# Kernel optimization log

Hardware: AMD Instinct MI355X
Metric: run time of the kernel (lower is better)

Reference implementation:

```python
import jax, jax.numpy as jnp
import numpy as np

KS = 16
FREQ = jnp.array([0., 1., 2., 4., 8., 16., 32., 64.], dtype=jnp.float32)  # [0]+[2^i], d=8
TWO_PI = 2.0 * np.pi


def softplus_b10(x):
    # torch F.softplus(x, beta=10, threshold=1): linear when beta*x > threshold
    bx = 10.0 * x
    return jnp.where(bx > 1.0, x, jnp.log1p(jnp.exp(jnp.minimum(bx, 1.0))) / 10.0)


def grid_sample_2d(img, gx, gy):
    # img: (C, H, W) complex; gx,gy: (N,) in [-1,1]. Bilinear, align_corners=True,
    # zero padding -- matches torch.nn.functional.grid_sample. Returns (C, N).
    C, H, W = img.shape
    ix = (gx + 1.0) * 0.5 * (W - 1)
    iy = (gy + 1.0) * 0.5 * (H - 1)
    ix0 = jnp.floor(ix)
    iy0 = jnp.floor(iy)
    wx = ix - ix0
    wy = iy - iy0

    def corner(iyc, ixc, w):
        valid = (ixc >= 0) & (ixc <= W - 1) & (iyc >= 0) & (iyc <= H - 1)
        ii = jnp.clip(ixc, 0, W - 1).astype(jnp.int32)
        jj = jnp.clip(iyc, 0, H - 1).astype(jnp.int32)
        return img[:, jj, ii] * (w * valid)[None, :]

    return (corner(iy0, ix0, (1 - wx) * (1 - wy))
            + corner(iy0, ix0 + 1, wx * (1 - wy))
            + corner(iy0 + 1, ix0, (1 - wx) * wy)
            + corner(iy0 + 1, ix0 + 1, wx * wy))


def batch_irfft(P, x):
    # P: (ks, d, N) complex; x: (N,) in [-1,1]. Trig-weighted inverse rFFT reduce.
    xx = (x + 1.0) * 0.5
    ang = TWO_PI * xx[:, None] * FREQ[None, :]            # (N, d)
    scale = jnp.where(FREQ > 0, 2.0, 1.0)
    c = jnp.cos(ang) * scale
    s = jnp.sin(ang) * scale
    return jnp.einsum('kdn,nd->kn', P.real, c) - jnp.einsum('kdn,nd->kn', P.imag, s)


def reference(xyz, bound, alpha_params, Pu_re, Pu_im, Pv_re, Pv_im, Pw_re, Pw_im):
    alpha = softplus_b10(alpha_params)[0]
    Pu = jnp.fft.ifftn((Pu_re + 1j * Pu_im) * alpha, axes=(3, 4))  # (1,ks,dx,Ny,Nz)
    Pv = jnp.fft.ifftn((Pv_re + 1j * Pv_im) * alpha, axes=(2, 4))  # (1,ks,Nx,dy,Nz)
    Pw = jnp.fft.ifftn((Pw_re + 1j * Pw_im) * alpha, axes=(2, 3))  # (1,ks,Nx,Ny,dz)

    xyzn = xyz / bound
    xs, ys, zs = xyzn[:, 0], xyzn[:, 1], xyzn[:, 2]
    N = xs.shape[0]

    ks, dx = Pu.shape[1], Pu.shape[2]
    dy = Pv.shape[3]
    dz = Pw.shape[4]

    # Pu: sample over (Ny, Nz) plane; grid (x=zs -> width Nz, y=ys -> height Ny)
    Px = grid_sample_2d(Pu[0].reshape(ks * dx, Pu.shape[3], Pu.shape[4]), zs, ys).reshape(ks, dx, N)
    # Pv: transpose (ks,Nx,dy,Nz)->(ks,dy,Nx,Nz); grid (x=zs -> Nz, y=xs -> Nx)
    Py = grid_sample_2d(jnp.swapaxes(Pv[0], 1, 2).reshape(ks * dy, Pv.shape[2], Pv.shape[4]), zs, xs).reshape(ks, dy, N)
    # Pw: transpose (ks,Nx,Ny,dz)->(ks,dz,Ny,Nx); grid (x=xs -> Nx, y=ys -> Ny)
    Pz = grid_sample_2d(jnp.swapaxes(Pw[0], 1, 3).reshape(ks * dz, Pw.shape[3], Pw.shape[2]), xs, ys).reshape(ks, dz, N)

    P = batch_irfft(Px, xs) + batch_irfft(Py, ys) + batch_irfft(Pz, zs)  # (ks, N)
    return P.T  # (N, ks)


def setup_inputs() -> dict:
    key = jax.random.key(0)
    ks = jax.random.split(key, 8)
    N = 131072
    xyz = jax.random.uniform(ks[0], (N, 3), dtype=jnp.float32, minval=-1.0, maxval=1.0)
    scale = 0.05
    return {
        'xyz': xyz,
        'bound': 1.0,
        'alpha_params': jnp.full((1,), 0.001, dtype=jnp.float32),
        'Pu_re': scale * jax.random.normal(ks[1], (1, KS, 8, 160, 160), dtype=jnp.float32),
        'Pu_im': scale * jax.random.normal(ks[2], (1, KS, 8, 160, 160), dtype=jnp.float32),
        'Pv_re': scale * jax.random.normal(ks[3], (1, KS, 160, 8, 160), dtype=jnp.float32),
        'Pv_im': scale * jax.random.normal(ks[4], (1, KS, 160, 8, 160), dtype=jnp.float32),
        'Pw_re': scale * jax.random.normal(ks[5], (1, KS, 160, 160, 8), dtype=jnp.float32),
        'Pw_im': scale * jax.random.normal(ks[6], (1, KS, 160, 160, 8), dtype=jnp.float32),
    }
```

## Files before the change

kernel.cpp:

```cpp
#include <hip/hip_runtime.h>
#include <hip/hip_bf16.h>

#define G 160
#define GM1 159
#define KD 128
#define KP 320
#define PLANE_U 3276800
#define NBUCK 32768
#define TWO_PI_F 6.28318530717958647692f

typedef __attribute__((ext_vector_type(8))) short bf16x8;
typedef __attribute__((ext_vector_type(4))) float f32x4;

__device__ __forceinline__ unsigned short f2bf(float x) {
    unsigned u = __float_as_uint(x);
    unsigned r = (u + 0x7FFFu + ((u >> 16) & 1u)) >> 16;
    return (unsigned short)r;
}
__device__ __forceinline__ unsigned int packbf(float re, float im) {
    union { __hip_bfloat162 h; unsigned int u; } cv;
    cv.h = __float22bfloat162_rn(make_float2(re, im));
    return cv.u;
}
__device__ __forceinline__ float bfl(unsigned u) { return __uint_as_float(u << 16); }
__device__ __forceinline__ float bfh(unsigned u) { return __uint_as_float(u & 0xffff0000u); }
__device__ __forceinline__ unsigned int wim_of(unsigned int u) {
    return ((u << 16) | (u >> 16)) ^ 0x00008000u;
}
__device__ __forceinline__ unsigned part1by2(unsigned x) {
    x &= 0x3FF;
    x = (x | (x << 16)) & 0xFF0000FFu;
    x = (x | (x << 8))  & 0x0300F00Fu;
    x = (x | (x << 4))  & 0x030C30C3u;
    x = (x | (x << 2))  & 0x09249249u;
    return x;
}
__device__ __forceinline__ unsigned morton_key(float x, float y, float z) {
    int cx = min(max((int)((x + 1.0f) * 16.0f), 0), 31);
    int cy = min(max((int)((y + 1.0f) * 16.0f), 0), 31);
    int cz = min(max((int)((z + 1.0f) * 16.0f), 0), 31);
    return part1by2(cx) | (part1by2(cy) << 1) | (part1by2(cz) << 2);
}

__global__ void k_init_w(unsigned short* __restrict__ Wre) {
    int idx = blockIdx.x * blockDim.x + threadIdx.x;
    if (idx >= G * KP) return;
    int r = idx / KP, kp = idx - r * KP;
    int q = kp >> 1;
    int m = (r * q) % G;
    float th = (float)m * (TWO_PI_F / (float)G);
    float s, c;
    __sincosf(th, &s, &c);
    Wre[idx] = f2bf(((kp & 1) == 0 ? c : -s) * (1.0f / (float)G));
}

__global__ void k_zero(unsigned int* __restrict__ counts) {
    int i = blockIdx.x * blockDim.x + threadIdx.x;
    if (i < NBUCK) counts[i] = 0;
}

__global__ __launch_bounds__(256) void k_hist(
    const float* __restrict__ xyz, const float* __restrict__ bound,
    unsigned int* __restrict__ counts, int N)
{
    int i = blockIdx.x * blockDim.x + threadIdx.x;
    if (i >= N) return;
    float invb = 1.0f / bound[0];
    float x = xyz[3 * i + 0] * invb;
    float y = xyz[3 * i + 1] * invb;
    float z = xyz[3 * i + 2] * invb;
    atomicAdd(&counts[morton_key(x, y, z)], 1u);
}

__global__ __launch_bounds__(1024) void k_scan(
    const unsigned int* __restrict__ counts,
    unsigned int* __restrict__ cursors)
{
    __shared__ unsigned int sT[1024];
    int t = threadIdx.x;
    unsigned int local[32];
    unsigned int s = 0;
    #pragma unroll
    for (int i = 0; i < 32; i++) { local[i] = counts[t * 32 + i]; s += local[i]; }
    sT[t] = s;
    __syncthreads();
    for (int off = 1; off < 1024; off <<= 1) {
        unsigned int v = (t >= off) ? sT[t - off] : 0u;
        __syncthreads();
        sT[t] += v;
        __syncthreads();
    }
    unsigned int run = (t > 0) ? sT[t - 1] : 0u;
    #pragma unroll
    for (int i = 0; i < 32; i++) { cursors[t * 32 + i] = run; run += local[i]; }
}

__global__ __launch_bounds__(256) void k_scatter(
    const float* __restrict__ xyz, const float* __restrict__ bound,
    unsigned int* __restrict__ cursors, float4* __restrict__ sxyz, int N)
{
    int i = blockIdx.x * blockDim.x + threadIdx.x;
    if (i >= N) return;
    float invb = 1.0f / bound[0];
    float x = xyz[3 * i + 0] * invb;
    float y = xyz[3 * i + 1] * invb;
    float z = xyz[3 * i + 2] * invb;
    unsigned int pos = atomicAdd(&cursors[morton_key(x, y, z)], 1u);
    sxyz[pos] = make_float4(x, y, z, __int_as_float(i));
}

__global__ __launch_bounds__(256) void k_packw(
    const float* __restrict__ Are, const float* __restrict__ Aim,
    unsigned int* __restrict__ Apw)
{
    __shared__ unsigned int sT[64 * 33];
    int k  = blockIdx.x;
    int pc = blockIdx.y;
    int q0 = blockIdx.z * 32;
    int tid = threadIdx.x;

    int i = tid & 63, qo = tid >> 6;
    size_t base = (size_t)k * 204800 + (size_t)pc * 64 + i;
    #pragma unroll
    for (int qc = 0; qc < 8; qc++) {
        int q = q0 + qo * 8 + qc;
        float r  = Are[base + (size_t)q * 1280];
        float im = Aim[base + (size_t)q * 1280];
        sT[i * 33 + qo * 8 + qc] = packbf(r, im);
    }
    __syncthreads();
    int qp = tid & 31, mo = tid >> 5;
    #pragma unroll
    for (int mc = 0; mc < 8; mc++) {
        int m = (k * 8 + mo) * G + pc * 8 + mc;
        Apw[(size_t)m * G + q0 + qp] = sT[(mc * 8 + mo) * 33 + qp];
    }
}

__global__ __launch_bounds__(512) void k_stage1(
    const float* __restrict__ Pu_re, const float* __restrict__ Pu_im,
    const float* __restrict__ Pv_re, const float* __restrict__ Pv_im,
    const unsigned int* __restrict__ Apw,
    const float* __restrict__ alpha_params,
    const unsigned short* __restrict__ Wre,
    unsigned int* __restrict__ Bfrag)
{
    int tid = threadIdx.x;
    int w = tid >> 6, lane = tid & 63;
    int col = lane & 15, g4 = lane >> 4;
    int gw = blockIdx.x * 8 + w;
    int mt0 = gw * 2;
    int plane = mt0 / 1280;
    int mtl0 = mt0 - plane * 1280;

    float ap = alpha_params[0];
    float bxv = 10.0f * ap;
    float alpha = (bxv > 1.0f) ? ap : log1pf(expf(fminf(bxv, 1.0f))) * 0.1f;

    bf16x8 afr[2][10];
    #pragma unroll
    for (int ti = 0; ti < 2; ti++) {
        int mtl = mtl0 + ti;
        if (plane == 2) {
            const unsigned int* a2 = Apw + (size_t)(mtl * 16 + col) * G + g4 * 4;
            #pragma unroll
            for (int t = 0; t < 10; t++) {
                union { uint4 u; bf16x8 b; } cv;
                cv.u = *(const uint4*)(a2 + t * 16);
                afr[ti][t] = cv.b;
            }
        } else {
            const float *Ar, *Ai; int sd_, sp_;
            if (plane == 0) { Ar = Pu_re; Ai = Pu_im; sd_ = 25600; sp_ = 160; }
            else            { Ar = Pv_re; Ai = Pv_im; sd_ = 160;   sp_ = 1280; }
            int m = mtl * 16 + col;
            int k = m / 1280; int rm = m - k * 1280;
            int d = rm / 160; int p = rm - d * 160;
            size_t abase = (size_t)k * 204800 + (size_t)d * sd_ + (size_t)p * sp_ + g4 * 4;
            #pragma unroll
            for (int t = 0; t < 10; t++) {
                float4 vr = *(const float4*)(Ar + abase + t * 16);
                float4 vi = *(const float4*)(Ai + abase + t * 16);
                union { unsigned int u[4]; bf16x8 b; } cv;
                cv.u[0] = packbf(vr.x, vi.x); cv.u[1] = packbf(vr.y, vi.y);
                cv.u[2] = packbf(vr.z, vi.z); cv.u[3] = packbf(vr.w, vi.w);
                afr[ti][t] = cv.b;
            }
        }
    }

    unsigned int* Bpl = Bfrag + (size_t)plane * PLANE_U;
    int kd0 = mtl0 / 10, pt0 = mtl0 - kd0 * 10;
    int mtl1 = mtl0 + 1;
    int kd1 = mtl1 / 10, pt1 = mtl1 - kd1 * 10;

    for (int lt = 0; lt < 10; lt++) {
        f32x4 ar0 = (f32x4)(0.f), ai0 = (f32x4)(0.f);
        f32x4 ar1 = (f32x4)(0.f), ai1 = (f32x4)(0.f);
        const unsigned short* wp = &Wre[(lt * 16 + col) * KP + g4 * 8];
        #pragma unroll
        for (int t = 0; t < 10; t++) {
            union { uint4 u; bf16x8 b; } cr, ci;
            cr.u = *(const uint4*)(wp + t * 32);
            ci.u.x = wim_of(cr.u.x); ci.u.y = wim_of(cr.u.y);
            ci.u.z = wim_of(cr.u.z); ci.u.w = wim_of(cr.u.w);
            ar0 = __builtin_amdgcn_mfma_f32_16x16x32_bf16(afr[0][t], cr.b, ar0, 0, 0, 0);
            ai0 = __builtin_amdgcn_mfma_f32_16x16x32_bf16(afr[0][t], ci.b, ai0, 0, 0, 0);
            ar1 = __builtin_amdgcn_mfma_f32_16x16x32_bf16(afr[1][t], cr.b, ar1, 0, 0, 0);
            ai1 = __builtin_amdgcn_mfma_f32_16x16x32_bf16(afr[1][t], ci.b, ai1, 0, 0, 0);
        }
        uint4 o0, o1;
        o0.x = packbf(alpha * ar0[0], alpha * ai0[0]);
        o0.y = packbf(alpha * ar0[1], alpha * ai0[1]);
        o0.z = packbf(alpha * ar0[2], alpha * ai0[2]);
        o0.w = packbf(alpha * ar0[3], alpha * ai0[3]);
        o1.x = packbf(alpha * ar1[0], alpha * ai1[0]);
        o1.y = packbf(alpha * ar1[1], alpha * ai1[1]);
        o1.z = packbf(alpha * ar1[2], alpha * ai1[2]);
        o1.w = packbf(alpha * ar1[3], alpha * ai1[3]);
        *(uint4*)(Bpl + (size_t)(kd0 * 10 + lt) * 2560 + pt0 * 256 + lane * 4) = o0;
        *(uint4*)(Bpl + (size_t)(kd1 * 10 + lt) * 2560 + pt1 * 256 + lane * 4) = o1;
    }
}

__global__ __launch_bounds__(640) void k_stage2(
    const unsigned int* __restrict__ Bfrag,
    const unsigned short* __restrict__ Wre,
    unsigned int* __restrict__ Tall)
{
    __shared__ __align__(16) unsigned int sB[20480];
    int tid = threadIdx.x;
    int w = tid >> 6, lane = tid & 63;
    int col = lane & 15, g4 = lane >> 4;
    int kdo = blockIdx.x;
    int lt  = blockIdx.y;
    int plane = blockIdx.z;

    const unsigned int* Bp = Bfrag + (size_t)plane * PLANE_U;
    #pragma unroll
    for (int i = 0; i < 8; i++) {
        uint4 v = *(const uint4*)(Bp + ((size_t)(kdo * 8 + i) * 10 + lt) * 2560 + tid * 4);
        *(uint4*)(sB + i * 2560 + tid * 4) = v;
    }

    bf16x8 wfr[10];
    const unsigned short* wp = &Wre[(w * 16 + col) * KP + g4 * 8];
    #pragma unroll
    for (int t = 0; t < 10; t++)
        wfr[t] = *(const bf16x8*)(wp + t * 32);

    __syncthreads();

    f32x4 ar[8], ai[8];
    #pragma unroll
    for (int i = 0; i < 8; i++) { ar[i] = (f32x4)(0.f); ai[i] = (f32x4)(0.f); }

    #pragma unroll
    for (int t = 0; t < 10; t++) {
        union { bf16x8 b; uint4 u; } cr, ci;
        cr.b = wfr[t];
        ci.u.x = wim_of(cr.u.x); ci.u.y = wim_of(cr.u.y);
        ci.u.z = wim_of(cr.u.z); ci.u.w = wim_of(cr.u.w);
        #pragma unroll
        for (int kq = 0; kq < 8; kq++) {
            bf16x8 bf = *(const bf16x8*)&sB[kq * 2560 + (t * 64 + lane) * 4];
            ar[kq] = __builtin_amdgcn_mfma_f32_16x16x32_bf16(cr.b, bf, ar[kq], 0, 0, 0);
            ai[kq] = __builtin_amdgcn_mfma_f32_16x16x32_bf16(ci.b, bf, ai[kq], 0, 0, 0);
        }
    }

    unsigned int* Tp = Tall + (size_t)plane * PLANE_U;
    #pragma unroll
    for (int reg = 0; reg < 4; reg++) {
        int j = w * 16 + g4 * 4 + reg;
        int l = lt * 16 + col;
        uint4 o0, o1;
        o0.x = packbf(ar[0][reg], ai[0][reg]);
        o0.y = packbf(ar[1][reg], ai[1][reg]);
        o0.z = packbf(ar[2][reg], ai[2][reg]);
        o0.w = packbf(ar[3][reg], ai[3][reg]);
        o1.x = packbf(ar[4][reg], ai[4][reg]);
        o1.y = packbf(ar[5][reg], ai[5][reg]);
        o1.z = packbf(ar[6][reg], ai[6][reg]);
        o1.w = packbf(ar[7][reg], ai[7][reg]);
        size_t ta = ((size_t)(j * G + l)) * KD + kdo * 8;
        *(uint4*)(Tp + ta)     = o0;
        *(uint4*)(Tp + ta + 4) = o1;
    }
}

__device__ __forceinline__ float plane_eval16(const unsigned int* __restrict__ T,
                                              float gy, float gx, float fc, int k)
{
    float iy = (gy + 1.0f) * 0.5f * (float)GM1;
    float ix = (gx + 1.0f) * 0.5f * (float)GM1;
    float iy0f = floorf(iy), ix0f = floorf(ix);
    float wy = iy - iy0f, wx = ix - ix0f;
    int iy0 = (int)iy0f, ix0 = (int)ix0f;
    int iy1 = min(iy0 + 1, GM1), ix1 = min(ix0 + 1, GM1);
    iy0 = max(min(iy0, GM1), 0); ix0 = max(min(ix0, GM1), 0);
    iy1 = max(iy1, 0); ix1 = max(ix1, 0);

    const unsigned int* c00 = &T[(size_t)(iy0 * G + ix0) * KD + k * 8];
    const unsigned int* c01 = &T[(size_t)(iy0 * G + ix1) * KD + k * 8];
    const unsigned int* c10 = &T[(size_t)(iy1 * G + ix0) * KD + k * 8];
    const unsigned int* c11 = &T[(size_t)(iy1 * G + ix1) * KD + k * 8];
    uint4 a00 = *(const uint4*)c00, b00 = *(const uint4*)(c00 + 4);
    uint4 a01 = *(const uint4*)c01, b01 = *(const uint4*)(c01 + 4);
    uint4 a10 = *(const uint4*)c10, b10 = *(const uint4*)(c10 + 4);
    uint4 a11 = *(const uint4*)c11, b11 = *(const uint4*)(c11 + 4);

    float w00 = (1.f - wx) * (1.f - wy), w01 = wx * (1.f - wy);
    float w10 = (1.f - wx) * wy,        w11 = wx * wy;

    float s1v, c1v;
    __sincosf(TWO_PI_F * fc, &s1v, &c1v);
    float cd[8], sd[8];
    cd[1] = c1v; sd[1] = s1v;
    #pragma unroll
    for (int d = 2; d < 8; d++) {
        float t2 = cd[d - 1] + cd[d - 1];
        cd[d] = __builtin_fmaf(t2, cd[d - 1], -1.0f);
        sd[d] = t2 * sd[d - 1];
    }

    float acc = 0.f;
#define TERM(u0, u1, u2, u3, C, S) { \
    float re = bfl(u0) * w00 + bfl(u1) * w01 + bfl(u2) * w10 + bfl(u3) * w11; \
    float im = bfh(u0) * w00 + bfh(u1) * w01 + bfh(u2) * w10 + bfh(u3) * w11; \
    acc += re * (C) - im * (S); }
    TERM(a00.x, a01.x, a10.x, a11.x, 1.0f, 0.0f)
    TERM(a00.y, a01.y, a10.y, a11.y, cd[1] + cd[1], sd[1] + sd[1])
    TERM(a00.z, a01.z, a10.z, a11.z, cd[2] + cd[2], sd[2] + sd[2])
    TERM(a00.w, a01.w, a10.w, a11.w, cd[3] + cd[3], sd[3] + sd[3])
    TERM(b00.x, b01.x, b10.x, b11.x, cd[4] + cd[4], sd[4] + sd[4])
    TERM(b00.y, b01.y, b10.y, b11.y, cd[5] + cd[5], sd[5] + sd[5])
    TERM(b00.z, b01.z, b10.z, b11.z, cd[6] + cd[6], sd[6] + sd[6])
    TERM(b00.w, b01.w, b10.w, b11.w, cd[7] + cd[7], sd[7] + sd[7])
#undef TERM
    return acc;
}

__global__ __launch_bounds__(256) void k_sample(
    const float4* __restrict__ sxyz,
    const unsigned int* __restrict__ Tu, const unsigned int* __restrict__ Tv,
    const unsigned int* __restrict__ Tw,
    float* __restrict__ out, int N)
{
    int tid = threadIdx.x;
    int k = tid & 15;
    int nblocks = (N + 15) / 16;
    int seg = blockIdx.x & 7;
    int segblocks = nblocks >> 3;
    int pid = (seg * segblocks + (blockIdx.x >> 3)) * 16 + (tid >> 4);
    if (pid >= N) return;

    float4 pw = sxyz[pid];
    int n = __float_as_int(pw.w);
    float x = pw.x, y = pw.y, z = pw.z;
    float xx = (x + 1.0f) * 0.5f;
    float yy = (y + 1.0f) * 0.5f;
    float zz = (z + 1.0f) * 0.5f;

    float acc = plane_eval16(Tu, y, z, xx, k)
              + plane_eval16(Tv, x, z, yy, k)
              + plane_eval16(Tw, y, x, zz, k);
    out[n * 16 + k] = acc;
}

extern "C" void kernel_launch(void* const* d_in, const int* in_sizes, int n_in,
                              void* d_out, int out_size, void* d_ws, size_t ws_size,
                              hipStream_t stream) {
    const float* xyz          = (const float*)d_in[0];
    const float* bound        = (const float*)d_in[1];
    const float* alpha_params = (const float*)d_in[2];
    const float* Pu_re = (const float*)d_in[3];
    const float* Pu_im = (const float*)d_in[4];
    const float* Pv_re = (const float*)d_in[5];
    const float* Pv_im = (const float*)d_in[6];
    const float* Pw_re = (const float*)d_in[7];
    const float* Pw_im = (const float*)d_in[8];
    float* out = (float*)d_out;
    int N = in_sizes[0] / 3;

    char* ws = (char*)d_ws;
    unsigned short* Wre  = (unsigned short*)(ws);
    unsigned int*   Apw  = (unsigned int*)(ws + 102400);
    unsigned int*   Bfr  = (unsigned int*)(ws + 102400 + 13107200);
    unsigned int*   Tall = (unsigned int*)(ws + 102400 + 13107200 + 39321600);
    char*           ws2  = ws + 102400 + 13107200 + 39321600 + 39321600;
    unsigned int*   counts  = (unsigned int*)(ws2);
    unsigned int*   cursors = (unsigned int*)(ws2 + 131072);
    float4*         sxyz    = (float4*)(ws2 + 262144);
    unsigned int*   Tu   = Tall;
    unsigned int*   Tv   = Tall + (size_t)PLANE_U;
    unsigned int*   Tw   = Tall + (size_t)2 * PLANE_U;

    k_zero<<<NBUCK / 256, 256, 0, stream>>>(counts);
    k_hist<<<(N + 255) / 256, 256, 0, stream>>>(xyz, bound, counts, N);
    k_scan<<<1, 1024, 0, stream>>>(counts, cursors);
    k_scatter<<<(N + 255) / 256, 256, 0, stream>>>(xyz, bound, cursors, sxyz, N);

    k_init_w<<<(G * KP + 255) / 256, 256, 0, stream>>>(Wre);
    k_packw<<<dim3(16, 20, 5), 256, 0, stream>>>(Pw_re, Pw_im, Apw);
    k_stage1<<<240, 512, 0, stream>>>(Pu_re, Pu_im, Pv_re, Pv_im, Apw,
                                      alpha_params, Wre, Bfr);
    k_stage2<<<dim3(16, 10, 3), 640, 0, stream>>>(Bfr, Wre, Tall);

    k_sample<<<(N + 15) / 16, 256, 0, stream>>>(sxyz, Tu, Tv, Tw, out, N);
}
```

Measured before the change: 263.2 us.

## Merge prep kernels, coarsen Morton buckets, batch all gather loads in sampler

Folds the bucket zeroing, twiddle-table init and Pw packing kernels into one launch to cut launch overhead. Coarsens the Morton sort grid from 32^3 to 16^3 buckets, which shrinks the histogram and scan but makes the sort less local. Restructures the sampler so all twelve corner loads for the three planes are issued before any arithmetic, which raises memory-level parallelism. It also adds a launch-bounds occupancy hint, and the extra live registers could lower occupancy or cause spills.

After: 262.0 us. No clear change (-0.4%).

```diff
diff --git a/kernel.cpp b/kernel.cpp
--- a/kernel.cpp
+++ b/kernel.cpp
@@ -6,7 +6,7 @@
 #define KD 128
 #define KP 320
 #define PLANE_U 3276800
-#define NBUCK 32768
+#define NBUCK 4096
 #define TWO_PI_F 6.28318530717958647692f
 
 typedef __attribute__((ext_vector_type(8))) short bf16x8;
@@ -36,27 +36,57 @@
     return x;
 }
 __device__ __forceinline__ unsigned morton_key(float x, float y, float z) {
-    int cx = min(max((int)((x + 1.0f) * 16.0f), 0), 31);
-    int cy = min(max((int)((y + 1.0f) * 16.0f), 0), 31);
-    int cz = min(max((int)((z + 1.0f) * 16.0f), 0), 31);
+    int cx = min(max((int)((x + 1.0f) * 8.0f), 0), 15);
+    int cy = min(max((int)((y + 1.0f) * 8.0f), 0), 15);
+    int cz = min(max((int)((z + 1.0f) * 8.0f), 0), 15);
     return part1by2(cx) | (part1by2(cy) << 1) | (part1by2(cz) << 2);
 }
 
-__global__ void k_init_w(unsigned short* __restrict__ Wre) {
-    int idx = blockIdx.x * blockDim.x + threadIdx.x;
-    if (idx >= G * KP) return;
-    int r = idx / KP, kp = idx - r * KP;
-    int q = kp >> 1;
-    int m = (r * q) % G;
-    float th = (float)m * (TWO_PI_F / (float)G);
-    float s, c;
-    __sincosf(th, &s, &c);
-    Wre[idx] = f2bf(((kp & 1) == 0 ? c : -s) * (1.0f / (float)G));
-}
-
-__global__ void k_zero(unsigned int* __restrict__ counts) {
-    int i = blockIdx.x * blockDim.x + threadIdx.x;
-    if (i < NBUCK) counts[i] = 0;
+__global__ __launch_bounds__(256) void k_prep(
+    const float* __restrict__ Pw_re, const float* __restrict__ Pw_im,
+    unsigned int* __restrict__ Apw, unsigned short* __restrict__ Wre,
+    unsigned int* __restrict__ counts)
+{
+    __shared__ unsigned int sT[64 * 33];
+    int b = blockIdx.x;
+    int tid = threadIdx.x;
+    if (b < 16) {
+        counts[b * 256 + tid] = 0;
+        return;
+    }
+    if (b < 216) {
+        int idx = (b - 16) * 256 + tid;
+        int r = idx / KP, kp = idx - r * KP;
+        int q = kp >> 1;
+        int m = (r * q) % G;
+        float th = (float)m * (TWO_PI_F / (float)G);
+        float s, c;
+        __sincosf(th, &s, &c);
+        Wre[idx] = f2bf(((kp & 1) == 0 ? c : -s) * (1.0f / (float)G));
+        return;
+    }
+    int b2 = b - 216;
+    int k  = b2 / 100;
+    int rem = b2 - k * 100;
+    int pc = rem / 5;
+    int q0 = (rem - pc * 5) * 32;
+
+    int i = tid & 63, qo = tid >> 6;
+    size_t base = (size_t)k * 204800 + (size_t)pc * 64 + i;
+    #pragma unroll
+    for (int qc = 0; qc < 8; qc++) {
+        int q = q0 + qo * 8 + qc;
+        float r  = Pw_re[base + (size_t)q * 1280];
+        float im = Pw_im[base + (size_t)q * 1280];
+        sT[i * 33 + qo * 8 + qc] = packbf(r, im);
+    }
+    __syncthreads();
+    int qp = tid & 31, mo = tid >> 5;
+    #pragma unroll
+    for (int mc = 0; mc < 8; mc++) {
+        int m = (k * 8 + mo) * G + pc * 8 + mc;
+        Apw[(size_t)m * G + q0 + qp] = sT[(mc * 8 + mo) * 33 + qp];
+    }
 }
 
 __global__ __launch_bounds__(256) void k_hist(
@@ -78,10 +108,10 @@
 {
     __shared__ unsigned int sT[1024];
     int t = threadIdx.x;
-    unsigned int local[32];
+    unsigned int local[4];
     unsigned int s = 0;
     #pragma unroll
-    for (int i = 0; i < 32; i++) { local[i] = counts[t * 32 + i]; s += local[i]; }
+    for (int i = 0; i < 4; i++) { local[i] = counts[t * 4 + i]; s += local[i]; }
     sT[t] = s;
     __syncthreads();
     for (int off = 1; off < 1024; off <<= 1) {
@@ -92,7 +122,7 @@
     }
     unsigned int run = (t > 0) ? sT[t - 1] : 0u;
     #pragma unroll
-    for (int i = 0; i < 32; i++) { cursors[t * 32 + i] = run; run += local[i]; }
+    for (int i = 0; i < 4; i++) { cursors[t * 4 + i] = run; run += local[i]; }
 }
 
 __global__ __launch_bounds__(256) void k_scatter(
@@ -107,34 +137,6 @@
     float z = xyz[3 * i + 2] * invb;
     unsigned int pos = atomicAdd(&cursors[morton_key(x, y, z)], 1u);
     sxyz[pos] = make_float4(x, y, z, __int_as_float(i));
-}
-
-__global__ __launch_bounds__(256) void k_packw(
-    const float* __restrict__ Are, const float* __restrict__ Aim,
-    unsigned int* __restrict__ Apw)
-{
-    __shared__ unsigned int sT[64 * 33];
-    int k  = blockIdx.x;
-    int pc = blockIdx.y;
-    int q0 = blockIdx.z * 32;
-    int tid = threadIdx.x;
-
-    int i = tid & 63, qo = tid >> 6;
-    size_t base = (size_t)k * 204800 + (size_t)pc * 64 + i;
-    #pragma unroll
-    for (int qc = 0; qc < 8; qc++) {
-        int q = q0 + qo * 8 + qc;
-        float r  = Are[base + (size_t)q * 1280];
-        float im = Aim[base + (size_t)q * 1280];
-        sT[i * 33 + qo * 8 + qc] = packbf(r, im);
-    }
-    __syncthreads();
-    int qp = tid & 31, mo = tid >> 5;
-    #pragma unroll
-    for (int mc = 0; mc < 8; mc++) {
-        int m = (k * 8 + mo) * G + pc * 8 + mc;
-        Apw[(size_t)m * G + q0 + qp] = sT[(mc * 8 + mo) * 33 + qp];
-    }
 }
 
 __global__ __launch_bounds__(512) void k_stage1(
@@ -289,30 +291,31 @@
     }
 }
 
-__device__ __forceinline__ float plane_eval16(const unsigned int* __restrict__ T,
-                                              float gy, float gx, float fc, int k)
-{
-    float iy = (gy + 1.0f) * 0.5f * (float)GM1;
-    float ix = (gx + 1.0f) * 0.5f * (float)GM1;
+__device__ __forceinline__ void plane_addr(const unsigned int* __restrict__ T,
+    float gy, float gx, int k, const unsigned int** cp, float* wv)
+{
+    float iy = (gy + 1.0f) * (0.5f * (float)GM1);
+    float ix = (gx + 1.0f) * (0.5f * (float)GM1);
     float iy0f = floorf(iy), ix0f = floorf(ix);
     float wy = iy - iy0f, wx = ix - ix0f;
     int iy0 = (int)iy0f, ix0 = (int)ix0f;
     int iy1 = min(iy0 + 1, GM1), ix1 = min(ix0 + 1, GM1);
     iy0 = max(min(iy0, GM1), 0); ix0 = max(min(ix0, GM1), 0);
     iy1 = max(iy1, 0); ix1 = max(ix1, 0);
-
-    const unsigned int* c00 = &T[(size_t)(iy0 * G + ix0) * KD + k * 8];
-    const unsigned int* c01 = &T[(size_t)(iy0 * G + ix1) * KD + k * 8];
-    const unsigned int* c10 = &T[(size_t)(iy1 * G + ix0) * KD + k * 8];
-    const unsigned int* c11 = &T[(size_t)(iy1 * G + ix1) * KD + k * 8];
-    uint4 a00 = *(const uint4*)c00, b00 = *(const uint4*)(c00 + 4);
-    uint4 a01 = *(const uint4*)c01, b01 = *(const uint4*)(c01 + 4);
-    uint4 a10 = *(const uint4*)c10, b10 = *(const uint4*)(c10 + 4);
-    uint4 a11 = *(const uint4*)c11, b11 = *(const uint4*)(c11 + 4);
-
-    float w00 = (1.f - wx) * (1.f - wy), w01 = wx * (1.f - wy);
-    float w10 = (1.f - wx) * wy,        w11 = wx * wy;
-
+    cp[0] = &T[(size_t)(iy0 * G + ix0) * KD + k * 8];
+    cp[1] = &T[(size_t)(iy0 * G + ix1) * KD + k * 8];
+    cp[2] = &T[(size_t)(iy1 * G + ix0) * KD + k * 8];
+    cp[3] = &T[(size_t)(iy1 * G + ix1) * KD + k * 8];
+    wv[0] = (1.f - wx) * (1.f - wy);
+    wv[1] = wx * (1.f - wy);
+    wv[2] = (1.f - wx) * wy;
+    wv[3] = wx * wy;
+}
+
+__device__ __forceinline__ float plane_math(const uint4* va, const uint4* vb,
+                                            const float* wv, float fc)
+{
+    float w00 = wv[0], w01 = wv[1], w10 = wv[2], w11 = wv[3];
     float s1v, c1v;
     __sincosf(TWO_PI_F * fc, &s1v, &c1v);
     float cd[8], sd[8];
@@ -323,25 +326,24 @@
         cd[d] = __builtin_fmaf(t2, cd[d - 1], -1.0f);
         sd[d] = t2 * sd[d - 1];
     }
-
     float acc = 0.f;
 #define TERM(u0, u1, u2, u3, C, S) { \
     float re = bfl(u0) * w00 + bfl(u1) * w01 + bfl(u2) * w10 + bfl(u3) * w11; \
     float im = bfh(u0) * w00 + bfh(u1) * w01 + bfh(u2) * w10 + bfh(u3) * w11; \
     acc += re * (C) - im * (S); }
-    TERM(a00.x, a01.x, a10.x, a11.x, 1.0f, 0.0f)
-    TERM(a00.y, a01.y, a10.y, a11.y, cd[1] + cd[1], sd[1] + sd[1])
-    TERM(a00.z, a01.z, a10.z, a11.z, cd[2] + cd[2], sd[2] + sd[2])
-    TERM(a00.w, a01.w, a10.w, a11.w, cd[3] + cd[3], sd[3] + sd[3])
-    TERM(b00.x, b01.x, b10.x, b11.x, cd[4] + cd[4], sd[4] + sd[4])
-    TERM(b00.y, b01.y, b10.y, b11.y, cd[5] + cd[5], sd[5] + sd[5])
-    TERM(b00.z, b01.z, b10.z, b11.z, cd[6] + cd[6], sd[6] + sd[6])
-    TERM(b00.w, b01.w, b10.w, b11.w, cd[7] + cd[7], sd[7] + sd[7])
+    TERM(va[0].x, va[1].x, va[2].x, va[3].x, 1.0f, 0.0f)
+    TERM(va[0].y, va[1].y, va[2].y, va[3].y, cd[1] + cd[1], sd[1] + sd[1])
+    TERM(va[0].z, va[1].z, va[2].z, va[3].z, cd[2] + cd[2], sd[2] + sd[2])
+    TERM(va[0].w, va[1].w, va[2].w, va[3].w, cd[3] + cd[3], sd[3] + sd[3])
+    TERM(vb[0].x, vb[1].x, vb[2].x, vb[3].x, cd[4] + cd[4], sd[4] + sd[4])
+    TERM(vb[0].y, vb[1].y, vb[2].y, vb[3].y, cd[5] + cd[5], sd[5] + sd[5])
+    TERM(vb[0].z, vb[1].z, vb[2].z, vb[3].z, cd[6] + cd[6], sd[6] + sd[6])
+    TERM(vb[0].w, vb[1].w, vb[2].w, vb[3].w, cd[7] + cd[7], sd[7] + sd[7])
 #undef TERM
     return acc;
 }
 
-__global__ __launch_bounds__(256) void k_sample(
+__global__ __launch_bounds__(256, 3) void k_sample(
     const float4* __restrict__ sxyz,
     const unsigned int* __restrict__ Tu, const unsigned int* __restrict__ Tv,
     const unsigned int* __restrict__ Tw,
@@ -358,13 +360,25 @@
     float4 pw = sxyz[pid];
     int n = __float_as_int(pw.w);
     float x = pw.x, y = pw.y, z = pw.z;
-    float xx = (x + 1.0f) * 0.5f;
-    float yy = (y + 1.0f) * 0.5f;
-    float zz = (z + 1.0f) * 0.5f;
-
-    float acc = plane_eval16(Tu, y, z, xx, k)
-              + plane_eval16(Tv, x, z, yy, k)
-              + plane_eval16(Tw, y, x, zz, k);
+
+    const unsigned int* cp[3][4];
+    float wv[3][4];
+    plane_addr(Tu, y, z, k, cp[0], wv[0]);
+    plane_addr(Tv, x, z, k, cp[1], wv[1]);
+    plane_addr(Tw, y, x, k, cp[2], wv[2]);
+
+    uint4 va[3][4], vb[3][4];
+    #pragma unroll
+    for (int pl = 0; pl < 3; pl++)
+        #pragma unroll
+        for (int c = 0; c < 4; c++) {
+            va[pl][c] = *(const uint4*)cp[pl][c];
+            vb[pl][c] = *(const uint4*)(cp[pl][c] + 4);
+        }
+
+    float acc = plane_math(va[0], vb[0], wv[0], (x + 1.0f) * 0.5f)
+              + plane_math(va[1], vb[1], wv[1], (y + 1.0f) * 0.5f)
+              + plane_math(va[2], vb[2], wv[2], (z + 1.0f) * 0.5f);
     out[n * 16 + k] = acc;
 }
 
@@ -390,22 +404,18 @@
     unsigned int*   Tall = (unsigned int*)(ws + 102400 + 13107200 + 39321600);
     char*           ws2  = ws + 102400 + 13107200 + 39321600 + 39321600;
     unsigned int*   counts  = (unsigned int*)(ws2);
-    unsigned int*   cursors = (unsigned int*)(ws2 + 131072);
-    float4*         sxyz    = (float4*)(ws2 + 262144);
+    unsigned int*   cursors = (unsigned int*)(ws2 + 16384);
+    float4*         sxyz    = (float4*)(ws2 + 32768);
     unsigned int*   Tu   = Tall;
     unsigned int*   Tv   = Tall + (size_t)PLANE_U;
     unsigned int*   Tw   = Tall + (size_t)2 * PLANE_U;
 
-    k_zero<<<NBUCK / 256, 256, 0, stream>>>(counts);
+    k_prep<<<1816, 256, 0, stream>>>(Pw_re, Pw_im, Apw, Wre, counts);
     k_hist<<<(N + 255) / 256, 256, 0, stream>>>(xyz, bound, counts, N);
     k_scan<<<1, 1024, 0, stream>>>(counts, cursors);
     k_scatter<<<(N + 255) / 256, 256, 0, stream>>>(xyz, bound, cursors, sxyz, N);
-
-    k_init_w<<<(G * KP + 255) / 256, 256, 0, stream>>>(Wre);
-    k_packw<<<dim3(16, 20, 5), 256, 0, stream>>>(Pw_re, Pw_im, Apw);
     k_stage1<<<240, 512, 0, stream>>>(Pu_re, Pu_im, Pv_re, Pv_im, Apw,
                                       alpha_params, Wre, Bfr);
     k_stage2<<<dim3(16, 10, 3), 640, 0, stream>>>(Bfr, Wre, Tall);
-
     k_sample<<<(N + 15) / 16, 256, 0, stream>>>(sxyz, Tu, Tv, Tw, out, N);
 }
```
